# Optimization experiments

Hardware: AMD Instinct MI355X
Metric: run time of the kernel (lower is better)

Reference implementation:

```python
import jax, jax.numpy as jnp
import numpy as np

N_NODES = 100000
N_EDGES = 1600000
IN_C, HID_C, OUT_C = 128, 128, 64


def setup_inputs() -> dict:
    key = jax.random.key(0)
    ks = jax.random.split(key, 8)
    x = jax.random.normal(ks[0], (N_NODES, IN_C), dtype=jnp.float32)
    edge_index = jax.random.randint(ks[1], (2, N_EDGES), 0, N_NODES, dtype=jnp.int32)
    # Glorot-ish init for GCNConv linear weights, zero bias (PyG default)
    def glorot(k, fan_in, fan_out):
        s = jnp.sqrt(6.0 / (fan_in + fan_out))
        return jax.random.uniform(k, (fan_in, fan_out), dtype=jnp.float32, minval=-s, maxval=s)
    return {
        "x": x,
        "edge_index": edge_index,
        "W1": glorot(ks[2], IN_C, HID_C), "b1": jnp.zeros((HID_C,), jnp.float32),
        "W2": glorot(ks[3], HID_C, HID_C), "b2": jnp.zeros((HID_C,), jnp.float32),
        "W3": glorot(ks[4], HID_C, OUT_C), "b3": jnp.zeros((OUT_C,), jnp.float32),
    }


def _gcn_norm(edge_index, num_nodes):
    # Add self-loops (PyG GCNConv default) and compute symmetric normalization
    loops = jnp.arange(num_nodes, dtype=edge_index.dtype)
    src = jnp.concatenate([edge_index[0], loops])  # [E+N]
    dst = jnp.concatenate([edge_index[1], loops])
    deg = jax.ops.segment_sum(jnp.ones_like(dst, dtype=jnp.float32), dst,
                              num_segments=num_nodes)
    deg_inv_sqrt = jnp.where(deg > 0, jax.lax.rsqrt(jnp.maximum(deg, 1.0)), 0.0)
    norm = deg_inv_sqrt[src] * deg_inv_sqrt[dst]  # [E+N]
    return src, dst, norm


def _gcn_layer(x, src, dst, norm, W, b, num_nodes):
    h = x @ W                                # [N, out] dense transform first
    msg = h[src] * norm[:, None]             # gather + scale  [E+N, out]
    out = jax.ops.segment_sum(msg, dst, num_segments=num_nodes)  # scatter-add
    return out + b


def reference(x, edge_index, W1, b1, W2, b2, W3, b3):
    n = x.shape[0]
    src, dst, norm = _gcn_norm(edge_index, n)
    h = jax.nn.relu(_gcn_layer(x, src, dst, norm, W1, b1, n))
    h = jax.nn.relu(_gcn_layer(h, src, dst, norm, W2, b2, n))
    return _gcn_layer(h, src, dst, norm, W3, b3, n)
```

## Files before the change

### kernel.cpp

```cpp
#include <hip/hip_runtime.h>

#define NN 100000
#define NE 1600000
#define NBK 391
#define BSH 8
#define MPAD 100096
#define SCB 391
#define CAP 5120
#define NB16 6250
#define G1B 1564

typedef unsigned short ushortT;
typedef unsigned long long ull;
using sh8 = __attribute__((ext_vector_type(8))) short;
using f4  = __attribute__((ext_vector_type(4))) float;


__device__ __forceinline__ unsigned short bfr(float f) {
  unsigned u = __float_as_uint(f);
  u += 0x7FFF + ((u >> 16) & 1);
  return (unsigned short)(u >> 16);
}
__device__ __forceinline__ float bf2f(unsigned short h) {
  return __uint_as_float(((unsigned)h) << 16);
}
__device__ __forceinline__ void acc8(const uint4 v, float* a) {
  a[0] += __uint_as_float(v.x << 16);
  a[1] += __uint_as_float(v.x & 0xFFFF0000u);
  a[2] += __uint_as_float(v.y << 16);
  a[3] += __uint_as_float(v.y & 0xFFFF0000u);
  a[4] += __uint_as_float(v.z << 16);
  a[5] += __uint_as_float(v.z & 0xFFFF0000u);
  a[6] += __uint_as_float(v.w << 16);
  a[7] += __uint_as_float(v.w & 0xFFFF0000u);
}
__device__ __forceinline__ void fma8(const uint4 v, const float s, float* a) {
  a[0] = fmaf(__uint_as_float(v.x << 16), s, a[0]);
  a[1] = fmaf(__uint_as_float(v.x & 0xFFFF0000u), s, a[1]);
  a[2] = fmaf(__uint_as_float(v.y << 16), s, a[2]);
  a[3] = fmaf(__uint_as_float(v.y & 0xFFFF0000u), s, a[3]);
  a[4] = fmaf(__uint_as_float(v.z << 16), s, a[4]);
  a[5] = fmaf(__uint_as_float(v.z & 0xFFFF0000u), s, a[5]);
  a[6] = fmaf(__uint_as_float(v.w << 16), s, a[6]);
  a[7] = fmaf(__uint_as_float(v.w & 0xFFFF0000u), s, a[7]);
}
__device__ __forceinline__ sh8 hi8(const float4 a, const float4 b) {
  sh8 r;
  r[0] = (short)bfr(a.x); r[1] = (short)bfr(a.y);
  r[2] = (short)bfr(a.z); r[3] = (short)bfr(a.w);
  r[4] = (short)bfr(b.x); r[5] = (short)bfr(b.y);
  r[6] = (short)bfr(b.z); r[7] = (short)bfr(b.w);
  return r;
}


template <int COUT>
__device__ __forceinline__ void packone(const float* __restrict__ W,
                                        ushortT* __restrict__ Bp, int i) {
  const int j = i & 7;
  const int l = (i >> 3) & 63;
  const int rest = i >> 9;
  const int g = rest % (COUT / 16);
  const int ks = rest / (COUT / 16);
  const int k = (ks & 3) * 32 + (l >> 4) * 8 + j;
  const int n = g * 16 + (l & 15);
  const float v = W[k * COUT + n];
  const unsigned short h = bfr(v);
  Bp[i] = (ks < 4) ? h : bfr(v - bf2f(h));
}


__global__ __launch_bounds__(256) void k_scatterpack(
    const int* __restrict__ src, const int* __restrict__ dst,
    int* __restrict__ cursor, unsigned* __restrict__ pairArr,
    const float* __restrict__ W1, const float* __restrict__ W2,
    const float* __restrict__ W3, ushortT* __restrict__ Bp1,
    ushortT* __restrict__ Bp2, ushortT* __restrict__ Bp3) {
  if (blockIdx.x >= SCB) {
    const int i = (blockIdx.x - SCB) * 256 + threadIdx.x;
    if (i < 32768) packone<128>(W1, Bp1, i);
    else if (i < 65536) packone<128>(W2, Bp2, i - 32768);
    else packone<64>(W3, Bp3, i - 65536);
    return;
  }
  __shared__ int lcnt[512];
  __shared__ int lbase[512];
  __shared__ int lrank[NBK];
  __shared__ int bbase[NBK];
  __shared__ int sd2[256];
  __shared__ unsigned sorted[4096];
  __shared__ int target[4096];
  const int t = threadIdx.x;
  for (int i = t; i < 512; i += 256) lcnt[i] = 0;
  for (int i = t; i < NBK; i += 256) lrank[i] = 0;
  __syncthreads();
  const int base = blockIdx.x * 4096;
  int rs[16], rd[16];
#pragma unroll
  for (int q = 0; q < 16; q++) {
    int e = base + t + 256 * q;
    rs[q] = (e < NE) ? src[e] : -1;
    rd[q] = (e < NE) ? dst[e] : -1;
    if (rd[q] >= 0) atomicAdd(&lcnt[rd[q] >> BSH], 1);
  }
  __syncthreads();
  const int s0 = lcnt[2 * t];
  const int s1 = lcnt[2 * t + 1];
  sd2[t] = s0 + s1;
  __syncthreads();
  for (int off = 1; off < 256; off <<= 1) {
    int x = (t >= off) ? sd2[t - off] : 0;
    __syncthreads();
    sd2[t] += x;
    __syncthreads();
  }
  const int epair = sd2[t] - (s0 + s1);
  lbase[2 * t] = epair;
  lbase[2 * t + 1] = epair + s0;
  __syncthreads();
  for (int i = t; i < NBK; i += 256)
    if (lcnt[i] > 0) bbase[i] = atomicAdd(&cursor[i], lcnt[i]);
  __syncthreads();
#pragma unroll
  for (int q = 0; q < 16; q++) {
    if (rd[q] >= 0) {
      int b = rd[q] >> BSH;
      int r = atomicAdd(&lrank[b], 1);
      int slot = lbase[b] + r;
      sorted[slot] = ((unsigned)rs[q] << 8) | ((unsigned)rd[q] & 255u);
      target[slot] = b * CAP + bbase[b] + r;
    }
  }
  __syncthreads();
  const int n = min(4096, NE - base);
  for (int s = t; s < n; s += 256) pairArr[target[s]] = sorted[s];
}


__global__ __launch_bounds__(256) void k_csrgemm1(
    const unsigned* __restrict__ pairArr, const int* __restrict__ cnt,
    float* __restrict__ dinv, int* __restrict__ rowptr, int* __restrict__ col,
    const float* __restrict__ X, const ushortT* __restrict__ Bp,
    ushortT* __restrict__ hs) {
  __shared__ int lc[256];
  __shared__ int sd[256];
  __shared__ int bc[NBK];
  const int t = threadIdx.x;
  if (blockIdx.x < NBK) {
    const int b = blockIdx.x;
    const int n0 = b << BSH;
    for (int i = t; i < NBK; i += 256) bc[i] = cnt[i];
    lc[t] = 0;
    __syncthreads();
    int partial = 0;
    for (int i = t; i < b; i += 256) partial += bc[i];
    sd[t] = partial;
    __syncthreads();
    for (int off = 128; off > 0; off >>= 1) {
      if (t < off) sd[t] += sd[t + off];
      __syncthreads();
    }
    const int ebeg = sd[0];
    const int myCnt = bc[b];
    __syncthreads();
    const unsigned* pb = pairArr + (size_t)b * CAP;
    for (int i = t; i < myCnt; i += 256)
      atomicAdd(&lc[pb[i] & 255u], 1);
    __syncthreads();
    const int v = lc[t];
    sd[t] = v;
    __syncthreads();
    for (int off = 1; off < 256; off <<= 1) {
      int x = (t >= off) ? sd[t - off] : 0;
      __syncthreads();
      sd[t] += x;
      __syncthreads();
    }
    const int excl = sd[t] - v;
    lc[t] = excl;
    const int node = n0 + t;
    if (node < NN) {
      rowptr[node] = ebeg + excl;
      dinv[node] = rsqrtf(1.0f + (float)v);
    }
    if (b == 0 && t == 0) rowptr[NN] = NE;
    __syncthreads();
    for (int i = t; i < myCnt; i += 256) {
      unsigned p = pb[i];
      int d = (int)(p & 255u);
      int srcv = (int)(p >> 8);
      int pos = atomicAdd(&lc[d], 1);
      col[ebeg + pos] = srcv;
    }
    return;
  }
  constexpr int CGALL = 8;
  constexpr int RG = 2;
  constexpr int CG = 4;
  const int bid = blockIdx.x - NBK;
  const int w = t >> 6;
  const int lane = t & 63;
  const int q = lane >> 4;
  const int c = lane & 15;
  const int row0 = bid * 64 + (w & 1) * 32;
  const int cg0 = (w >> 1) * 4;

  const float* xp[RG];
#pragma unroll
  for (int rg = 0; rg < RG; rg++) {
    const int row = row0 + rg * 16 + c;
    xp[rg] = X + (size_t)min(row, NN - 1) * 128 + q * 8;
  }
  const ushortT* bp0 = Bp + (size_t)lane * 8;

  f4 acc[RG][CG];
#pragma unroll
  for (int i = 0; i < RG; i++)
#pragma unroll
    for (int j = 0; j < CG; j++) acc[i][j] = (f4){0.f, 0.f, 0.f, 0.f};

  sh8 ah[RG], bh[CG], bl[CG];
  sh8 nah[RG], nbh[CG], nbl[CG];

  auto loadA = [&](int kr, sh8 (&h)[RG]) {
#pragma unroll
    for (int rg = 0; rg < RG; rg++) {
      const float4 x0 = *reinterpret_cast<const float4*>(xp[rg] + kr * 32);
      const float4 x1 = *reinterpret_cast<const float4*>(xp[rg] + kr * 32 + 4);
      h[rg] = hi8(x0, x1);
    }
  };
  auto loadB = [&](int kr, sh8 (&h)[CG], sh8 (&l)[CG]) {
#pragma unroll
    for (int cg = 0; cg < CG; cg++) {
      h[cg] = *reinterpret_cast<const sh8*>(bp0 + (size_t)(kr * CGALL + cg0 + cg) * 512);
      l[cg] = *reinterpret_cast<const sh8*>(bp0 + (size_t)((4 + kr) * CGALL + cg0 + cg) * 512);
    }
  };

  loadA(0, ah);
  loadB(0, bh, bl);
#pragma unroll
  for (int kr = 0; kr < 4; kr++) {
    if (kr < 3) {
      loadA(kr + 1, nah);
      loadB(kr + 1, nbh, nbl);
    }
#pragma unroll
    for (int rg = 0; rg < RG; rg++)
#pragma unroll
      for (int cg = 0; cg < CG; cg++)
        acc[rg][cg] = __builtin_amdgcn_mfma_f32_16x16x32_bf16(ah[rg], bh[cg],
                                                              acc[rg][cg], 0, 0, 0);
#pragma unroll
    for (int rg = 0; rg < RG; rg++)
#pragma unroll
      for (int cg = 0; cg < CG; cg++)
        acc[rg][cg] = __builtin_amdgcn_mfma_f32_16x16x32_bf16(ah[rg], bl[cg],
                                                              acc[rg][cg], 0, 0, 0);
    if (kr < 3) {
#pragma unroll
      for (int rg = 0; rg < RG; rg++) ah[rg] = nah[rg];
#pragma unroll
      for (int cg = 0; cg < CG; cg++) { bh[cg] = nbh[cg]; bl[cg] = nbl[cg]; }
    }
  }

#pragma unroll
  for (int rg = 0; rg < RG; rg++) {
#pragma unroll
    for (int reg = 0; reg < 4; reg++) {
      const int row = row0 + rg * 16 + q * 4 + reg;
      if (row < NN) {
#pragma unroll
        for (int cg = 0; cg < CG; cg++) {
          hs[(size_t)row * 128 + (cg0 + cg) * 16 + c] = bfr(acc[rg][cg][reg]);
        }
      }
    }
  }
}


template <int COUT, bool ESCALE>
__global__ __launch_bounds__(256, 6) void k_aggemm(
    const ushortT* __restrict__ hs_in, const int* __restrict__ rowptr,
    const int* __restrict__ col, const float* __restrict__ dinv,
    const float* __restrict__ bias, const ushortT* __restrict__ Bp,
    ushortT* __restrict__ hs_out) {
  constexpr int CGALL = COUT / 16;
  __shared__ ushortT At[4 * 512];
  const int t = threadIdx.x;
  const int w = t >> 6;
  const int lane = t & 63;
  const int q = lane >> 4;
  const int c = lane & 15;
  const int chb = c * 8;
  const int nw0 = blockIdx.x * 16 + w * 4;

  const int rpv = rowptr[min(nw0 + (lane & 7), NN)];
  const float dvv = dinv[min(nw0 + (lane & 3), NN - 1)];
  const float4 b0 = *reinterpret_cast<const float4*>(bias + chb);
  const float4 b1 = *reinterpret_cast<const float4*>(bias + chb + 4);
  char* const myAt = reinterpret_cast<char*>(At) + w * 1024;

  for (int it = 0; it < 4; ++it) {
    const int node = nw0 + it;
    const int beg = __shfl(rpv, it);
    const int end = __shfl(rpv, it + 1);
    const float di = __shfl(dvv, it);
    float a[8] = {};
    if (q == 0) {
      const uint4 v = *reinterpret_cast<const uint4*>(hs_in + (long)node * 128 + chb);
      if (ESCALE) fma8(v, di, a); else acc8(v, a);
    }
    int j = beg;
    if (j + 8 <= end) {
      int c0 = col[j + q];
      int c1 = col[j + 4 + q];
      float d0 = 0.f, d1 = 0.f;
      if (ESCALE) { d0 = dinv[c0]; d1 = dinv[c1]; }
      while (true) {
        const uint4 v0 = *reinterpret_cast<const uint4*>(hs_in + (long)c0 * 128 + chb);
        const uint4 v1 = *reinterpret_cast<const uint4*>(hs_in + (long)c1 * 128 + chb);
        j += 8;
        const bool more = (j + 8 <= end);
        int m0, m1;
        float e0 = 0.f, e1 = 0.f;
        if (more) {
          m0 = col[j + q]; m1 = col[j + 4 + q];
          if (ESCALE) { e0 = dinv[m0]; e1 = dinv[m1]; }
        }
        if (ESCALE) { fma8(v0, d0, a); fma8(v1, d1, a); }
        else { acc8(v0, a); acc8(v1, a); }
        if (!more) break;
        c0 = m0; c1 = m1; d0 = e0; d1 = e1;
      }
    }
    if (j + 4 <= end) {
      int cc = col[j + q];
      float ds = ESCALE ? dinv[cc] : 0.f;
      const uint4 v = *reinterpret_cast<const uint4*>(hs_in + (long)cc * 128 + chb);
      if (ESCALE) fma8(v, ds, a); else acc8(v, a);
      j += 4;
    }
    {
      const int rem = end - j;
      if (q < rem) {
        int cc = col[j + q];
        float ds = ESCALE ? dinv[cc] : 0.f;
        const uint4 v = *reinterpret_cast<const uint4*>(hs_in + (long)cc * 128 + chb);
        if (ESCALE) fma8(v, ds, a); else acc8(v, a);
      }
    }
#pragma unroll
    for (int i = 0; i < 8; i++) a[i] += __shfl(a[i], lane ^ 32);
#pragma unroll
    for (int i = 0; i < 8; i++) a[i] += __shfl(a[i], lane ^ 16);
    if (q == 0) {
      float o[8];
      o[0] = fmaf(a[0], di, b0.x); o[1] = fmaf(a[1], di, b0.y);
      o[2] = fmaf(a[2], di, b0.z); o[3] = fmaf(a[3], di, b0.w);
      o[4] = fmaf(a[4], di, b1.x); o[5] = fmaf(a[5], di, b1.y);
      o[6] = fmaf(a[6], di, b1.z); o[7] = fmaf(a[7], di, b1.w);
#pragma unroll
      for (int i = 0; i < 8; i++) o[i] = fmaxf(o[i], 0.f);
      uint4 H;
      H.x = (unsigned)bfr(o[0]) | ((unsigned)bfr(o[1]) << 16);
      H.y = (unsigned)bfr(o[2]) | ((unsigned)bfr(o[3]) << 16);
      H.z = (unsigned)bfr(o[4]) | ((unsigned)bfr(o[5]) << 16);
      H.w = (unsigned)bfr(o[6]) | ((unsigned)bfr(o[7]) << 16);
      *reinterpret_cast<uint4*>(myAt + ((unsigned)(it * 256 + c * 16) ^ (unsigned)(it << 4))) = H;
    }
  }
  asm volatile("s_waitcnt lgkmcnt(0)" ::: "memory");
  __builtin_amdgcn_sched_barrier(0);

  const ushortT* bp0 = Bp + (size_t)lane * 8;
  const int rr = c & 3;
  sh8 af[4];
#pragma unroll
  for (int kr = 0; kr < 4; ++kr) {
    const unsigned bo = (unsigned)((rr * 256 + kr * 64 + q * 16) ^ (rr << 4));
    af[kr] = *reinterpret_cast<const sh8*>(myAt + bo);
  }
  const float dvr0 = __shfl(dvv, 0), dvr1 = __shfl(dvv, 1),
              dvr2 = __shfl(dvv, 2), dvr3 = __shfl(dvv, 3);
#pragma unroll 1
  for (int ph = 0; ph < CGALL / 4; ++ph) {
    f4 acc[4];
#pragma unroll
    for (int u = 0; u < 4; ++u) acc[u] = (f4){0.f, 0.f, 0.f, 0.f};
#pragma unroll
    for (int kr = 0; kr < 4; ++kr) {
#pragma unroll
      for (int u = 0; u < 4; ++u) {
        const sh8 bh = *reinterpret_cast<const sh8*>(
            bp0 + (size_t)(kr * CGALL + ph * 4 + u) * 512);
        acc[u] = __builtin_amdgcn_mfma_f32_16x16x32_bf16(af[kr], bh, acc[u], 0, 0, 0);
      }
#pragma unroll
      for (int u = 0; u < 4; ++u) {
        const sh8 bl = *reinterpret_cast<const sh8*>(
            bp0 + (size_t)((4 + kr) * CGALL + ph * 4 + u) * 512);
        acc[u] = __builtin_amdgcn_mfma_f32_16x16x32_bf16(af[kr], bl, acc[u], 0, 0, 0);
      }
    }
    if (q == 0) {
#pragma unroll
      for (int u = 0; u < 4; ++u) {
        const int cc0 = (ph * 4 + u) * 16 + c;
        hs_out[(size_t)(nw0 + 0) * COUT + cc0] = bfr(acc[u][0] * dvr0);
        hs_out[(size_t)(nw0 + 1) * COUT + cc0] = bfr(acc[u][1] * dvr1);
        hs_out[(size_t)(nw0 + 2) * COUT + cc0] = bfr(acc[u][2] * dvr2);
        hs_out[(size_t)(nw0 + 3) * COUT + cc0] = bfr(acc[u][3] * dvr3);
      }
    }
  }
}


__global__ __launch_bounds__(256) void k_agg64(const ushortT* __restrict__ hs,
                                               const int* __restrict__ rowptr,
                                               const int* __restrict__ col,
                                               const float* __restrict__ dinv,
                                               const float* __restrict__ bias,
                                               float* __restrict__ out) {
  const int gid = blockIdx.x * 256 + threadIdx.x;
  const int node = gid >> 6;
  if (node >= NN) return;
  const int lane = threadIdx.x & 63;
  const int o8 = lane >> 3;
  const int chb = (lane & 7) * 8;
  const int beg = rowptr[node];
  const int end = rowptr[node + 1];

  float a[8] = {};
  if (o8 == 0) {
    const uint4 v = *reinterpret_cast<const uint4*>(hs + (long)node * 64 + chb);
    acc8(v, a);
  }

  int j = beg;
  if (j + 16 <= end) {
    int c0 = col[j + o8];
    int c1 = col[j + 8 + o8];
    while (true) {
      const uint4 v0 = *reinterpret_cast<const uint4*>(hs + (long)c0 * 64 + chb);
      const uint4 v1 = *reinterpret_cast<const uint4*>(hs + (long)c1 * 64 + chb);
      j += 16;
      const bool more = (j + 16 <= end);
      int n0, n1;
      if (more) { n0 = col[j + o8]; n1 = col[j + 8 + o8]; }
      acc8(v0, a);
      acc8(v1, a);
      if (!more) break;
      c0 = n0; c1 = n1;
    }
  }
  for (; j + 8 <= end; j += 8) {
    int c = col[j + o8];
    const uint4 v = *reinterpret_cast<const uint4*>(hs + (long)c * 64 + chb);
    acc8(v, a);
  }
  {
    const int r = end - j;
    if (o8 < r) {
      int c = col[j + o8];
      const uint4 v = *reinterpret_cast<const uint4*>(hs + (long)c * 64 + chb);
      acc8(v, a);
    }
  }

#pragma unroll
  for (int i = 0; i < 8; i++) a[i] += __shfl(a[i], lane ^ 32);
#pragma unroll
  for (int i = 0; i < 8; i++) a[i] += __shfl(a[i], lane ^ 16);
#pragma unroll
  for (int i = 0; i < 8; i++) a[i] += __shfl(a[i], lane ^ 8);

  if (o8 == 0) {
    const float di = dinv[node];
    const float4 b0 = *reinterpret_cast<const float4*>(bias + chb);
    const float4 b1 = *reinterpret_cast<const float4*>(bias + chb + 4);
    float4 r0, r1;
    r0.x = fmaf(a[0], di, b0.x); r0.y = fmaf(a[1], di, b0.y);
    r0.z = fmaf(a[2], di, b0.z); r0.w = fmaf(a[3], di, b0.w);
    r1.x = fmaf(a[4], di, b1.x); r1.y = fmaf(a[5], di, b1.y);
    r1.z = fmaf(a[6], di, b1.z); r1.w = fmaf(a[7], di, b1.w);
    *reinterpret_cast<float4*>(out + (long)node * 64 + chb) = r0;
    *reinterpret_cast<float4*>(out + (long)node * 64 + chb + 4) = r1;
  }
}


extern "C" void kernel_launch(void* const* d_in, const int* in_sizes, int n_in,
                              void* d_out, int out_size, void* d_ws, size_t ws_size,
                              hipStream_t stream) {
  const float* x  = (const float*)d_in[0];
  const int* ei   = (const int*)d_in[1];
  const float* W1 = (const float*)d_in[2];
  const float* b1 = (const float*)d_in[3];
  const float* W2 = (const float*)d_in[4];
  const float* b2 = (const float*)d_in[5];
  const float* W3 = (const float*)d_in[6];
  const float* b3 = (const float*)d_in[7];
  float* out = (float*)d_out;
  const int* srcp = ei;
  const int* dstp = ei + NE;

  char* wsb = (char*)d_ws;
  size_t off = 0;
  auto alloc = [&](size_t bytes) -> void* {
    void* p = wsb + off;
    off += (bytes + 255) & ~(size_t)255;
    return p;
  };
  ushortT* hs1 = (ushortT*)alloc((size_t)MPAD * 128 * 2);
  ushortT* hs2 = (ushortT*)alloc((size_t)NN * 128 * 2);
  int*   col    = (int*)alloc((size_t)NE * 4);
  int*   rowptr = (int*)alloc((size_t)(NN + 1) * 4);
  float* dinv   = (float*)alloc((size_t)NN * 4);
  int*   cursor = (int*)alloc((size_t)NBK * 4);
  ushortT* Bp1 = (ushortT*)alloc((size_t)32768 * 2);
  ushortT* Bp2 = (ushortT*)alloc((size_t)32768 * 2);
  ushortT* Bp3 = (ushortT*)alloc((size_t)16384 * 2);
  unsigned* pairArr = (unsigned*)hs2;
  ushortT* hs3 = hs1;
  (void)ws_size; (void)in_sizes; (void)n_in; (void)out_size;

  hipMemsetAsync(cursor, 0, (size_t)NBK * 4, stream);
  k_scatterpack<<<SCB + 320, 256, 0, stream>>>(srcp, dstp, cursor, pairArr,
                                               W1, W2, W3, Bp1, Bp2, Bp3);
  k_csrgemm1<<<NBK + G1B, 256, 0, stream>>>(pairArr, cursor, dinv, rowptr, col,
                                            x, Bp1, hs1);

  const int aggGrid = (NN * 64) / 256;

  k_aggemm<128, true><<<NB16, 256, 0, stream>>>(hs1, rowptr, col, dinv, b1, Bp2, hs2);
  k_aggemm<64, false><<<NB16, 256, 0, stream>>>(hs2, rowptr, col, dinv, b2, Bp3, hs3);
  k_agg64<<<aggGrid, 256, 0, stream>>>(hs3, rowptr, col, dinv, b3, out);
}
```

Before: 385.1 us.

## Share aggregated tile across block and split GEMM columns per wave

The fused aggregate+GEMM kernel used to have each wave run MFMAs on its own 4 nodes padded into a 16-row tile, redoing the full weight pass per wave. It now stores all 16 aggregated rows of the block in shared LDS, syncs the block, and gives each wave a quarter of the output columns over the full 16 rows. This removes the 4x redundant MFMA work and weight loads, and raises the occupancy hint from 6 to 8. In exchange it adds a block-wide barrier between the gather and the GEMM.

```diff
diff --git a/kernel.cpp b/kernel.cpp
--- a/kernel.cpp
+++ b/kernel.cpp
@@ -283,29 +283,31 @@
 
 
 template <int COUT, bool ESCALE>
-__global__ __launch_bounds__(256, 6) void k_aggemm(
+__global__ __launch_bounds__(256, 8) void k_aggemm(
     const ushortT* __restrict__ hs_in, const int* __restrict__ rowptr,
     const int* __restrict__ col, const float* __restrict__ dinv,
     const float* __restrict__ bias, const ushortT* __restrict__ Bp,
     ushortT* __restrict__ hs_out) {
   constexpr int CGALL = COUT / 16;
-  __shared__ ushortT At[4 * 512];
+  constexpr int UPW = CGALL / 4;
+  __shared__ ushortT At[16 * 128];
   const int t = threadIdx.x;
   const int w = t >> 6;
   const int lane = t & 63;
   const int q = lane >> 4;
   const int c = lane & 15;
   const int chb = c * 8;
-  const int nw0 = blockIdx.x * 16 + w * 4;
+  const int n0 = blockIdx.x * 16;
+  const int nw0 = n0 + w * 4;
 
   const int rpv = rowptr[min(nw0 + (lane & 7), NN)];
   const float dvv = dinv[min(nw0 + (lane & 3), NN - 1)];
   const float4 b0 = *reinterpret_cast<const float4*>(bias + chb);
   const float4 b1 = *reinterpret_cast<const float4*>(bias + chb + 4);
-  char* const myAt = reinterpret_cast<char*>(At) + w * 1024;
 
   for (int it = 0; it < 4; ++it) {
     const int node = nw0 + it;
+    const int r = w * 4 + it;
     const int beg = __shfl(rpv, it);
     const int end = __shfl(rpv, it + 1);
     const float di = __shfl(dvv, it);
@@ -339,7 +341,7 @@
     }
     if (j + 4 <= end) {
       int cc = col[j + q];
-      float ds = ESCALE ? dinv[cc] : 0.f;
+      const float ds = ESCALE ? dinv[cc] : 0.f;
       const uint4 v = *reinterpret_cast<const uint4*>(hs_in + (long)cc * 128 + chb);
       if (ESCALE) fma8(v, ds, a); else acc8(v, a);
       j += 4;
@@ -348,7 +350,7 @@
       const int rem = end - j;
       if (q < rem) {
         int cc = col[j + q];
-        float ds = ESCALE ? dinv[cc] : 0.f;
+        const float ds = ESCALE ? dinv[cc] : 0.f;
         const uint4 v = *reinterpret_cast<const uint4*>(hs_in + (long)cc * 128 + chb);
         if (ESCALE) fma8(v, ds, a); else acc8(v, a);
       }
@@ -370,51 +372,44 @@
       H.y = (unsigned)bfr(o[2]) | ((unsigned)bfr(o[3]) << 16);
       H.z = (unsigned)bfr(o[4]) | ((unsigned)bfr(o[5]) << 16);
       H.w = (unsigned)bfr(o[6]) | ((unsigned)bfr(o[7]) << 16);
-      *reinterpret_cast<uint4*>(myAt + ((unsigned)(it * 256 + c * 16) ^ (unsigned)(it << 4))) = H;
-    }
-  }
-  asm volatile("s_waitcnt lgkmcnt(0)" ::: "memory");
-  __builtin_amdgcn_sched_barrier(0);
-
+      const unsigned bo = (unsigned)(r * 256 + c * 16) ^ (unsigned)((r & 7) << 4);
+      *reinterpret_cast<uint4*>(reinterpret_cast<char*>(At) + bo) = H;
+    }
+  }
+  __syncthreads();
+
+  const int cg0 = w * UPW;
   const ushortT* bp0 = Bp + (size_t)lane * 8;
-  const int rr = c & 3;
-  sh8 af[4];
+  const char* ab = reinterpret_cast<const char*>(At);
+  const int arow = c;
+  f4 acc[UPW];
+#pragma unroll
+  for (int u = 0; u < UPW; ++u) acc[u] = (f4){0.f, 0.f, 0.f, 0.f};
 #pragma unroll
   for (int kr = 0; kr < 4; ++kr) {
-    const unsigned bo = (unsigned)((rr * 256 + kr * 64 + q * 16) ^ (rr << 4));
-    af[kr] = *reinterpret_cast<const sh8*>(myAt + bo);
-  }
-  const float dvr0 = __shfl(dvv, 0), dvr1 = __shfl(dvv, 1),
-              dvr2 = __shfl(dvv, 2), dvr3 = __shfl(dvv, 3);
-#pragma unroll 1
-  for (int ph = 0; ph < CGALL / 4; ++ph) {
-    f4 acc[4];
-#pragma unroll
-    for (int u = 0; u < 4; ++u) acc[u] = (f4){0.f, 0.f, 0.f, 0.f};
-#pragma unroll
-    for (int kr = 0; kr < 4; ++kr) {
-#pragma unroll
-      for (int u = 0; u < 4; ++u) {
-        const sh8 bh = *reinterpret_cast<const sh8*>(
-            bp0 + (size_t)(kr * CGALL + ph * 4 + u) * 512);
-        acc[u] = __builtin_amdgcn_mfma_f32_16x16x32_bf16(af[kr], bh, acc[u], 0, 0, 0);
-      }
-#pragma unroll
-      for (int u = 0; u < 4; ++u) {
-        const sh8 bl = *reinterpret_cast<const sh8*>(
-            bp0 + (size_t)((4 + kr) * CGALL + ph * 4 + u) * 512);
-        acc[u] = __builtin_amdgcn_mfma_f32_16x16x32_bf16(af[kr], bl, acc[u], 0, 0, 0);
-      }
-    }
-    if (q == 0) {
-#pragma unroll
-      for (int u = 0; u < 4; ++u) {
-        const int cc0 = (ph * 4 + u) * 16 + c;
-        hs_out[(size_t)(nw0 + 0) * COUT + cc0] = bfr(acc[u][0] * dvr0);
-        hs_out[(size_t)(nw0 + 1) * COUT + cc0] = bfr(acc[u][1] * dvr1);
-        hs_out[(size_t)(nw0 + 2) * COUT + cc0] = bfr(acc[u][2] * dvr2);
-        hs_out[(size_t)(nw0 + 3) * COUT + cc0] = bfr(acc[u][3] * dvr3);
-      }
+    const unsigned bo =
+        (unsigned)(arow * 256 + kr * 64 + q * 16) ^ (unsigned)((arow & 7) << 4);
+    const sh8 af = *reinterpret_cast<const sh8*>(ab + bo);
+#pragma unroll
+    for (int u = 0; u < UPW; ++u) {
+      const sh8 bh = *reinterpret_cast<const sh8*>(
+          bp0 + (size_t)(kr * CGALL + cg0 + u) * 512);
+      acc[u] = __builtin_amdgcn_mfma_f32_16x16x32_bf16(af, bh, acc[u], 0, 0, 0);
+    }
+#pragma unroll
+    for (int u = 0; u < UPW; ++u) {
+      const sh8 bl = *reinterpret_cast<const sh8*>(
+          bp0 + (size_t)((4 + kr) * CGALL + cg0 + u) * 512);
+      acc[u] = __builtin_amdgcn_mfma_f32_16x16x32_bf16(af, bl, acc[u], 0, 0, 0);
+    }
+  }
+#pragma unroll
+  for (int reg = 0; reg < 4; ++reg) {
+    const int row = n0 + q * 4 + reg;
+    const float dv = dinv[row];
+#pragma unroll
+    for (int u = 0; u < UPW; ++u) {
+      hs_out[(size_t)row * COUT + (cg0 + u) * 16 + c] = bfr(acc[u][reg] * dv);
     }
   }
 }
```

New measurement: 349.0 us. -9.4%, faster.
